# Kernel optimization log

Hardware: AMD Instinct MI355X
Metric: run time of the kernel (lower is better)

Reference implementation:

```python
import jax, jax.numpy as jnp
import numpy as np

B, S, D_MODEL = 4, 1024, 1024
N_HEAD, D_HEAD = 16, 64
ALL_HEAD = N_HEAD * D_HEAD
SCALE = 1.0 / (D_HEAD ** 0.5)
LN_EPS = 1e-5


def setup_inputs() -> dict:
    key = jax.random.key(0)
    ks = jax.random.split(key, 8)
    inp = jax.random.normal(ks[0], (B, S, D_MODEL), dtype=jnp.float32)
    attn_mask = jax.random.randint(ks[1], (B, S), 0, 2, dtype=jnp.int32)
    w = lambda k, shp: (jax.random.normal(k, shp, dtype=jnp.float32) * 0.02)
    Wq = w(ks[2], (D_MODEL, ALL_HEAD)); bq = jnp.zeros((ALL_HEAD,), jnp.float32)
    Wk = w(ks[3], (D_MODEL, ALL_HEAD)); bk = jnp.zeros((ALL_HEAD,), jnp.float32)
    Wv = w(ks[4], (D_MODEL, ALL_HEAD)); bv = jnp.zeros((ALL_HEAD,), jnp.float32)
    Wo = w(ks[5], (ALL_HEAD, D_MODEL))
    ln_g = jnp.ones((D_MODEL,), jnp.float32)
    ln_b = jnp.zeros((D_MODEL,), jnp.float32)
    return {"inp": inp, "attn_mask": attn_mask, "Wq": Wq, "bq": bq,
            "Wk": Wk, "bk": bk, "Wv": Wv, "bv": bv, "Wo": Wo,
            "ln_g": ln_g, "ln_b": ln_b}


def _layer_norm(x, g, b):
    mu = jnp.mean(x, axis=-1, keepdims=True)
    var = jnp.mean((x - mu) ** 2, axis=-1, keepdims=True)
    return (x - mu) * jax.lax.rsqrt(var + LN_EPS) * g + b


def reference(inp, attn_mask, Wq, bq, Wk, bk, Wv, bv, Wo, ln_g, ln_b):
    residual = inp
    # QKV projections -> [B, S, H, D] -> flat [B*H, S, D] (batch-major, as torch permute+reshape)
    def proj(W, bias):
        h = (inp @ W + bias).reshape(B, S, N_HEAD, D_HEAD)
        return h.transpose(0, 2, 1, 3).reshape(B * N_HEAD, S, D_HEAD)
    q = proj(Wq, bq)
    k = proj(Wk, bk)
    v = proj(Wv, bv)
    # scores [B*H, S, S]
    scores = jnp.einsum('bqd,bkd->bqk', q, k) * SCALE
    # key-padding mask: nonzero -> masked_fill(-100000.0)
    mask = (attn_mask.astype(scores.dtype) != 0)  # [B, S]
    mask = jnp.broadcast_to(mask[:, None, None, :], (B, N_HEAD, S, S))
    mask = mask.reshape(B * N_HEAD, S, S)
    scores = jnp.where(mask, jnp.float32(-100000.0), scores)
    probs = jax.nn.softmax(scores, axis=2)  # dropout is identity in eval
    attn_vec = jnp.einsum('bqk,bkd->bqd', probs, v)  # [B*H, S, D]
    # faithful to torch: view(n_head, B, S, d_head).permute(1,2,0,3)
    attn_vec = attn_vec.reshape(N_HEAD, B, S, D_HEAD).transpose(1, 2, 0, 3)
    attn_vec = attn_vec.reshape(B, S, ALL_HEAD)
    attn_out = attn_vec @ Wo  # o_net has no bias; output dropout identity
    # post-lnorm (pre_lnorm=False)
    return _layer_norm(residual + attn_out, ln_g, ln_b)
```

## Files before the change

### kernel.cpp

```cpp
#include <hip/hip_runtime.h>

typedef __attribute__((ext_vector_type(8))) short bf16x8;
typedef __attribute__((ext_vector_type(4))) float f32x4;
typedef __attribute__((ext_vector_type(16))) float f32x16;

#define D_MODEL 1024
#define SEQ 1024
#define NB 4
#define NH 16
#define DH 64
#define MROWS 4096

__device__ __forceinline__ unsigned short f2bf(float f) {
    union { float f; unsigned u; } x; x.f = f;
    unsigned r = x.u + 0x7fffu + ((x.u >> 16) & 1u);
    return (unsigned short)(r >> 16);
}

__device__ __forceinline__ float bf2f(unsigned short u) {
    union { unsigned u; float f; } x; x.u = (unsigned)u << 16;
    return x.f;
}

__device__ __forceinline__ void gload16(const void* g, void* l) {
    __builtin_amdgcn_global_load_lds((const __attribute__((address_space(1))) void*)g,
                                     (__attribute__((address_space(3))) void*)l, 16, 0, 0);
}

__device__ __forceinline__ float xhalf(float x, int hi) {
    float a = x, b = x;
    asm volatile("v_permlane32_swap_b32 %0, %1" : "+v"(a), "+v"(b));
    return hi ? b : a;
}

__global__ __launch_bounds__(256) void prep(const float* __restrict__ x,
                                            unsigned short* __restrict__ Xb,
                                            const int* __restrict__ amask,
                                            unsigned long long* __restrict__ mwords,
                                            const float* __restrict__ Wq,
                                            const float* __restrict__ Wk,
                                            const float* __restrict__ Wv,
                                            const float* __restrict__ Wo,
                                            unsigned short* __restrict__ Wqkv_t,
                                            unsigned short* __restrict__ Wo_t) {
    __shared__ float tile[32][33];
    const int bid = blockIdx.x, tid = threadIdx.x;
    if (bid < 4096) {
        int i = bid * 256 + tid;
        float4 v = ((const float4*)x)[i];
        ushort4 r;
        r.x = f2bf(v.x); r.y = f2bf(v.y); r.z = f2bf(v.z); r.w = f2bf(v.w);
        ((ushort4*)Xb)[i] = r;
    } else if (bid < 8192) {
        int t = bid - 4096;
        const int mtx = t >> 10, t10 = t & 1023;
        const float* src = mtx == 0 ? Wq : mtx == 1 ? Wk : mtx == 2 ? Wv : Wo;
        unsigned short* dst = mtx < 3 ? (Wqkv_t + (size_t)mtx * D_MODEL * D_MODEL) : Wo_t;
        const int n0 = (t10 & 31) * 32, k0 = (t10 >> 5) * 32;
        const int tx = tid & 31, ty = tid >> 5;
        #pragma unroll
        for (int i = 0; i < 32; i += 8)
            tile[ty + i][tx] = src[(size_t)(k0 + ty + i) * D_MODEL + n0 + tx];
        __syncthreads();
        #pragma unroll
        for (int i = 0; i < 32; i += 8)
            dst[(size_t)(n0 + ty + i) * D_MODEL + k0 + tx] = f2bf(tile[tx][ty + i]);
    } else {
        int word = (bid - 8192) * 4 + (tid >> 6);
        int lane = tid & 63;
        unsigned long long m = __ballot(amask[word * 64 + lane] != 0);
        if (lane == 0) mwords[word] = m;
    }
}

#define CSW(r, c) ((r) * 128 + ((c) ^ (((r) & 7) << 3)))

__global__ __launch_bounds__(256) void gemm_qkv(const unsigned short* __restrict__ Xb,
                                                const unsigned short* __restrict__ Wt,
                                                const float* __restrict__ bq,
                                                const float* __restrict__ bk,
                                                const float* __restrict__ bv,
                                                unsigned short* __restrict__ Qb,
                                                unsigned short* __restrict__ Kb,
                                                unsigned short* __restrict__ Vt) {
    __shared__ unsigned short SM[32768];
    const int tid = threadIdx.x;
    const int lane = tid & 63, wid = tid >> 6;
    const int fr = lane & 15, fg = lane >> 4;
    const int wr = wid >> 1, wc = wid & 1;
    const int lin = blockIdx.x;
    const int x = lin & 7, i = lin >> 3;
    const int bxm = (x & 3) * 8 + (i & 7);
    const int byn = (x >> 2) * 12 + (i >> 3);
    const int m0 = bxm * 128, n0 = byn * 128;
    const unsigned short* Ag = Xb + (size_t)m0 * D_MODEL;
    const unsigned short* Bg = Wt + (size_t)n0 * D_MODEL;
    const int srow = tid >> 3;
    const int scol = 8 * ((tid & 7) ^ ((tid >> 3) & 7));
    f32x4 acc[4][4] = {};

#define QSTAGE(bf, kt2)                                                                   \
    {                                                                                     \
        const int kb = (kt2) * 64;                                                        \
        _Pragma("unroll")                                                                 \
        for (int j = 0; j < 4; ++j) {                                                     \
            int row = j * 32 + srow;                                                      \
            gload16(Ag + (size_t)row * D_MODEL + kb + scol, &SM[(bf) * 16384 + (j * 256 + tid) * 8]); \
            gload16(Bg + (size_t)row * D_MODEL + kb + scol, &SM[(bf) * 16384 + 8192 + (j * 256 + tid) * 8]); \
        }                                                                                 \
    }

    QSTAGE(0, 0);
    __syncthreads();
    int buf = 0;
    for (int kt = 0; kt < 16; ++kt) {
        if (kt < 15) QSTAGE(buf ^ 1, kt + 1);
        const unsigned short* As = &SM[buf * 16384];
        const unsigned short* Bs = &SM[buf * 16384 + 8192];
        #pragma unroll
        for (int ks = 0; ks < 2; ++ks) {
            bf16x8 af[4], bfv[4];
            #pragma unroll
            for (int m = 0; m < 4; ++m) {
                int row = wr * 64 + m * 16 + fr;
                af[m] = *(const bf16x8*)&As[row * 64 + ((ks * 32 + fg * 8) ^ ((row & 7) * 8))];
            }
            #pragma unroll
            for (int n = 0; n < 4; ++n) {
                int row = wc * 64 + n * 16 + fr;
                bfv[n] = *(const bf16x8*)&Bs[row * 64 + ((ks * 32 + fg * 8) ^ ((row & 7) * 8))];
            }
            __builtin_amdgcn_s_setprio(1);
            #pragma unroll
            for (int m = 0; m < 4; ++m)
                #pragma unroll
                for (int n = 0; n < 4; ++n)
                    acc[m][n] = __builtin_amdgcn_mfma_f32_16x16x32_bf16(af[m], bfv[n], acc[m][n], 0, 0, 0);
            __builtin_amdgcn_s_setprio(0);
        }
        __syncthreads();
        buf ^= 1;
    }
#undef QSTAGE
    unsigned short* Cs = SM;
    const int sel = n0 >> 10;
    const int npb = n0 & 1023;
    if (sel < 2) {
        #pragma unroll
        for (int n = 0; n < 4; ++n) {
            int cn = wc * 64 + n * 16 + fr;
            float bias = (sel == 0 ? bq : bk)[npb + cn];
            #pragma unroll
            for (int m = 0; m < 4; ++m)
                #pragma unroll
                for (int r = 0; r < 4; ++r) {
                    int row = wr * 64 + m * 16 + fg * 4 + r;
                    Cs[CSW(row, cn)] = f2bf(acc[m][n][r] + bias);
                }
        }
        __syncthreads();
        unsigned short* dst = sel == 0 ? Qb : Kb;
        #pragma unroll
        for (int k = 0; k < 8; ++k) {
            int c = k * 256 + tid;
            int row = c >> 4, cc = c & 15;
            int np = npb + cc * 8;
            int h = np >> 6, d = np & 63;
            int gm = m0 + row, b = gm >> 10, s = gm & 1023;
            bf16x8 v = *(const bf16x8*)&Cs[CSW(row, cc * 8)];
            *(bf16x8*)&dst[((size_t)(b * NH + h) * SEQ + s) * DH + d] = v;
        }
    } else {
        #pragma unroll
        for (int n = 0; n < 4; ++n) {
            int cn = wc * 64 + n * 16 + fr;
            float bias = bv[npb + cn];
            #pragma unroll
            for (int m = 0; m < 4; ++m)
                #pragma unroll
                for (int r = 0; r < 4; ++r) {
                    int row = wr * 64 + m * 16 + fg * 4 + r;
                    Cs[CSW(cn, row)] = f2bf(acc[m][n][r] + bias);
                }
        }
        __syncthreads();
        #pragma unroll
        for (int k = 0; k < 8; ++k) {
            int c = k * 256 + tid;
            int dcol = c >> 4, scc = c & 15;
            int np = npb + dcol;
            int h = np >> 6, dd = np & 63;
            int gm0 = m0 + scc * 8, b = gm0 >> 10, s0 = gm0 & 1023;
            bf16x8 v = *(const bf16x8*)&Cs[CSW(dcol, scc * 8)];
            *(bf16x8*)&Vt[((size_t)(b * NH + h) * DH + dd) * SEQ + s0] = v;
        }
    }
}

__global__ __launch_bounds__(256) void gemm_o(const unsigned short* __restrict__ Ab,
                                              const unsigned short* __restrict__ Wt,
                                              unsigned short* __restrict__ tmpb) {
    __shared__ unsigned short SM[32768];
    const int tid = threadIdx.x;
    const int lane = tid & 63, wid = tid >> 6;
    const int fr = lane & 15, fg = lane >> 4;
    const int wr = wid >> 1, wc = wid & 1;
    const int lin = blockIdx.x;
    const int x = lin & 7, i = lin >> 3;
    const int bxm = (x & 3) * 8 + (i & 7);
    const int byn = (x >> 2) * 4 + (i >> 3);
    const int m0 = bxm * 128, n0 = byn * 128;
    const unsigned short* Ag = Ab + (size_t)m0 * D_MODEL;
    const unsigned short* Bg = Wt + (size_t)n0 * D_MODEL;
    const int srow = tid >> 3;
    const int scol = 8 * ((tid & 7) ^ ((tid >> 3) & 7));
    f32x4 acc[4][4] = {};

#define OSTAGE(bf, kt2)                                                                   \
    {                                                                                     \
        const int kb = (kt2) * 64;                                                        \
        _Pragma("unroll")                                                                 \
        for (int j = 0; j < 4; ++j) {                                                     \
            int row = j * 32 + srow;                                                      \
            gload16(Ag + (size_t)row * D_MODEL + kb + scol, &SM[(bf) * 16384 + (j * 256 + tid) * 8]); \
            gload16(Bg + (size_t)row * D_MODEL + kb + scol, &SM[(bf) * 16384 + 8192 + (j * 256 + tid) * 8]); \
        }                                                                                 \
    }

    OSTAGE(0, 0);
    __syncthreads();
    int buf = 0;
    for (int kt = 0; kt < 16; ++kt) {
        if (kt < 15) OSTAGE(buf ^ 1, kt + 1);
        const unsigned short* As = &SM[buf * 16384];
        const unsigned short* Bs = &SM[buf * 16384 + 8192];
        #pragma unroll
        for (int ks = 0; ks < 2; ++ks) {
            bf16x8 af[4], bfv[4];
            #pragma unroll
            for (int m = 0; m < 4; ++m) {
                int row = wr * 64 + m * 16 + fr;
                af[m] = *(const bf16x8*)&As[row * 64 + ((ks * 32 + fg * 8) ^ ((row & 7) * 8))];
            }
            #pragma unroll
            for (int n = 0; n < 4; ++n) {
                int row = wc * 64 + n * 16 + fr;
                bfv[n] = *(const bf16x8*)&Bs[row * 64 + ((ks * 32 + fg * 8) ^ ((row & 7) * 8))];
            }
            __builtin_amdgcn_s_setprio(1);
            #pragma unroll
            for (int m = 0; m < 4; ++m)
                #pragma unroll
                for (int n = 0; n < 4; ++n)
                    acc[m][n] = __builtin_amdgcn_mfma_f32_16x16x32_bf16(af[m], bfv[n], acc[m][n], 0, 0, 0);
            __builtin_amdgcn_s_setprio(0);
        }
        __syncthreads();
        buf ^= 1;
    }
#undef OSTAGE
    unsigned short* Cs = SM;
    #pragma unroll
    for (int n = 0; n < 4; ++n) {
        int cn = wc * 64 + n * 16 + fr;
        #pragma unroll
        for (int m = 0; m < 4; ++m)
            #pragma unroll
            for (int r = 0; r < 4; ++r) {
                int row = wr * 64 + m * 16 + fg * 4 + r;
                Cs[CSW(row, cn)] = f2bf(acc[m][n][r]);
            }
    }
    __syncthreads();
    #pragma unroll
    for (int k = 0; k < 8; ++k) {
        int c = k * 256 + tid;
        int row = c >> 4, cc = c & 15;
        bf16x8 v = *(const bf16x8*)&Cs[CSW(row, cc * 8)];
        *(bf16x8*)&tmpb[(size_t)(m0 + row) * D_MODEL + n0 + cc * 8] = v;
    }
}

__global__ __launch_bounds__(256, 2) void attn_kernel(const unsigned short* __restrict__ Qb,
                                                      const unsigned short* __restrict__ Kb,
                                                      const unsigned short* __restrict__ Vt,
                                                      const unsigned long long* __restrict__ mwords,
                                                      unsigned short* __restrict__ AF) {
    __shared__ unsigned short Ks[2][128 * 64];
    __shared__ unsigned short Vts[2][64 * 128];
    const int tid = threadIdx.x, lane = tid & 63, wid = tid >> 6;
    const int l31 = lane & 31, hi = lane >> 5;
    const int lin = blockIdx.x;
    const int x = lin & 7, i = lin >> 3;
    const int qt = i & 7, bh = x * 8 + (i >> 3);
    const int b = bh >> 4;
    const unsigned short* Qh = Qb + (size_t)bh * SEQ * DH;
    const unsigned short* Kh = Kb + (size_t)bh * SEQ * DH;
    const unsigned short* Vth = Vt + (size_t)bh * DH * SEQ;
    const unsigned long long* mwb = mwords + b * 16;
    const int q0 = qt * 128 + wid * 32;

    const int k_row = wid * 32 + (lane >> 3);
    const int k_col = 8 * ((lane & 7) ^ ((lane >> 3) & 7));
    const int v_rowb = wid * 16 + (lane >> 4);

    bf16x8 qf[4];
    #pragma unroll
    for (int ks = 0; ks < 4; ++ks)
        qf[ks] = *(const bf16x8*)(Qh + (size_t)(q0 + l31) * DH + ks * 16 + hi * 8);

    union U4 { unsigned u[4]; bf16x8 v; };
    U4 ones;
    ones.u[0] = 0x3F803F80u; ones.u[1] = 0x3F803F80u;
    ones.u[2] = 0x3F803F80u; ones.u[3] = 0x3F803F80u;

    f32x16 oacc0 = {}, oacc1 = {};
    f32x16 sacc = {};
    float mrun = -3.0e38f;
    const float C2 = 0.18033688f;

#define KSWZ(row, colsh) ((row) * 64 + ((colsh) ^ (((row) & 7) << 3)))
#define VSWZ(row, colsh) ((row) * 128 + ((colsh) ^ (((row) & 7) << 3)))
#define STAGE(bufi, kt2)                                                                  \
    {                                                                                     \
        const int kv0s = (kt2) * 128;                                                     \
        _Pragma("unroll")                                                                 \
        for (int j = 0; j < 4; ++j)                                                       \
            gload16(Kh + (size_t)(kv0s + k_row + j * 8) * DH + k_col,                     \
                    &Ks[bufi][wid * 2048 + j * 512]);                                     \
        _Pragma("unroll")                                                                 \
        for (int j = 0; j < 4; ++j) {                                                     \
            const int vr = v_rowb + j * 4;                                                \
            gload16(Vth + (size_t)vr * SEQ + kv0s + 8 * ((lane & 15) ^ (vr & 7)),         \
                    &Vts[bufi][wid * 2048 + j * 512]);                                    \
        }                                                                                 \
    }

    STAGE(0, 0);
    __syncthreads();
    int buf = 0;
    for (int kt = 0; kt < 8; ++kt) {
        if (kt < 7) STAGE(buf ^ 1, kt + 1);
        const unsigned long long mwA = mwb[2 * kt], mwB = mwb[2 * kt + 1];
        const unsigned mr0 = (unsigned)mwA, mr1 = (unsigned)(mwA >> 32);
        const unsigned mr2 = (unsigned)mwB, mr3 = (unsigned)(mwB >> 32);
        f32x16 sA0 = {}, sA1 = {}, sB0 = {}, sB1 = {};
        __builtin_amdgcn_s_setprio(1);
        #pragma unroll
        for (int ks = 0; ks < 4; ++ks) {
            const int ch = ks * 16 + hi * 8;
            bf16x8 k0 = *(const bf16x8*)&Ks[buf][KSWZ(l31, ch)];
            bf16x8 k1 = *(const bf16x8*)&Ks[buf][KSWZ(32 + l31, ch)];
            bf16x8 k2 = *(const bf16x8*)&Ks[buf][KSWZ(64 + l31, ch)];
            bf16x8 k3 = *(const bf16x8*)&Ks[buf][KSWZ(96 + l31, ch)];
            sA0 = __builtin_amdgcn_mfma_f32_32x32x16_bf16(k0, qf[ks], sA0, 0, 0, 0);
            sA1 = __builtin_amdgcn_mfma_f32_32x32x16_bf16(k1, qf[ks], sA1, 0, 0, 0);
            sB0 = __builtin_amdgcn_mfma_f32_32x32x16_bf16(k2, qf[ks], sB0, 0, 0, 0);
            sB1 = __builtin_amdgcn_mfma_f32_32x32x16_bf16(k3, qf[ks], sB1, 0, 0, 0);
        }
        {
            U4 ab; ab.u[1] = 0; ab.u[2] = 0; ab.u[3] = 0;
            unsigned bv;
            bv = ((mr0 >> l31) & 1u) ? 0xC943u : 0u; ab.u[0] = hi ? 0u : bv;
            sA0 = __builtin_amdgcn_mfma_f32_32x32x16_bf16(ab.v, ones.v, sA0, 0, 0, 0);
            bv = ((mr1 >> l31) & 1u) ? 0xC943u : 0u; ab.u[0] = hi ? 0u : bv;
            sA1 = __builtin_amdgcn_mfma_f32_32x32x16_bf16(ab.v, ones.v, sA1, 0, 0, 0);
            bv = ((mr2 >> l31) & 1u) ? 0xC943u : 0u; ab.u[0] = hi ? 0u : bv;
            sB0 = __builtin_amdgcn_mfma_f32_32x32x16_bf16(ab.v, ones.v, sB0, 0, 0, 0);
            bv = ((mr3 >> l31) & 1u) ? 0xC943u : 0u; ab.u[0] = hi ? 0u : bv;
            sB1 = __builtin_amdgcn_mfma_f32_32x32x16_bf16(ab.v, ones.v, sB1, 0, 0, 0);
        }
        __builtin_amdgcn_s_setprio(0);
        float tm[16];
        #pragma unroll
        for (int r2 = 0; r2 < 16; ++r2)
            tm[r2] = fmaxf(fmaxf(sA0[r2], sA1[r2]), fmaxf(sB0[r2], sB1[r2]));
        #pragma unroll
        for (int st = 8; st; st >>= 1)
            #pragma unroll
            for (int r2 = 0; r2 < st; ++r2)
                tm[r2] = fmaxf(tm[r2], tm[r2 + st]);
        float m = tm[0];
        m = fmaxf(m, xhalf(m, hi));
        float mt = m * C2;
        if (!__all(mt <= mrun + 11.5f)) {
            float newm = fmaxf(mrun, mt);
            float corr = exp2f(mrun - newm);
            #pragma unroll
            for (int r2 = 0; r2 < 16; ++r2) {
                oacc0[r2] *= corr; oacc1[r2] *= corr; sacc[r2] *= corr;
            }
            mrun = newm;
        }
        #pragma unroll
        for (int r2 = 0; r2 < 16; ++r2) {
            sA0[r2] = exp2f(fmaf(sA0[r2], C2, -mrun));
            sA1[r2] = exp2f(fmaf(sA1[r2], C2, -mrun));
            sB0[r2] = exp2f(fmaf(sB0[r2], C2, -mrun));
            sB1[r2] = exp2f(fmaf(sB1[r2], C2, -mrun));
        }
        unsigned cA0[8], cA1[8], cB0[8], cB1[8];
        #pragma unroll
        for (int ii = 0; ii < 8; ++ii) {
            asm volatile("v_cvt_pk_bf16_f32 %0, %1, %2" : "=v"(cA0[ii]) : "v"(sA0[2 * ii]), "v"(sA0[2 * ii + 1]));
            asm volatile("v_cvt_pk_bf16_f32 %0, %1, %2" : "=v"(cA1[ii]) : "v"(sA1[2 * ii]), "v"(sA1[2 * ii + 1]));
            asm volatile("v_cvt_pk_bf16_f32 %0, %1, %2" : "=v"(cB0[ii]) : "v"(sB0[2 * ii]), "v"(sB0[2 * ii + 1]));
            asm volatile("v_cvt_pk_bf16_f32 %0, %1, %2" : "=v"(cB1[ii]) : "v"(sB1[2 * ii]), "v"(sB1[2 * ii + 1]));
        }
        #pragma unroll
        for (int g = 0; g < 8; g += 4) {
            asm volatile("v_permlane32_swap_b32 %0, %1" : "+v"(cA0[g + 0]), "+v"(cA0[g + 2]));
            asm volatile("v_permlane32_swap_b32 %0, %1" : "+v"(cA0[g + 1]), "+v"(cA0[g + 3]));
            asm volatile("v_permlane32_swap_b32 %0, %1" : "+v"(cA1[g + 0]), "+v"(cA1[g + 2]));
            asm volatile("v_permlane32_swap_b32 %0, %1" : "+v"(cA1[g + 1]), "+v"(cA1[g + 3]));
            asm volatile("v_permlane32_swap_b32 %0, %1" : "+v"(cB0[g + 0]), "+v"(cB0[g + 2]));
            asm volatile("v_permlane32_swap_b32 %0, %1" : "+v"(cB0[g + 1]), "+v"(cB0[g + 3]));
            asm volatile("v_permlane32_swap_b32 %0, %1" : "+v"(cB1[g + 0]), "+v"(cB1[g + 2]));
            asm volatile("v_permlane32_swap_b32 %0, %1" : "+v"(cB1[g + 1]), "+v"(cB1[g + 3]));
        }
        __builtin_amdgcn_s_setprio(1);
        #pragma unroll
        for (int t = 0; t < 8; ++t) {
            const unsigned* cp = (t < 2) ? cA0 : (t < 4) ? cA1 : (t < 6) ? cB0 : cB1;
            const int g = (t & 1) * 4;
            U4 pb;
            pb.u[0] = cp[g + 0]; pb.u[1] = cp[g + 1]; pb.u[2] = cp[g + 2]; pb.u[3] = cp[g + 3];
            const int ch = t * 16 + hi * 8;
            bf16x8 vf0 = *(const bf16x8*)&Vts[buf][VSWZ(l31, ch)];
            bf16x8 vf1 = *(const bf16x8*)&Vts[buf][VSWZ(32 + l31, ch)];
            oacc0 = __builtin_amdgcn_mfma_f32_32x32x16_bf16(vf0, pb.v, oacc0, 0, 0, 0);
            oacc1 = __builtin_amdgcn_mfma_f32_32x32x16_bf16(vf1, pb.v, oacc1, 0, 0, 0);
            sacc  = __builtin_amdgcn_mfma_f32_32x32x16_bf16(ones.v, pb.v, sacc, 0, 0, 0);
        }
        __builtin_amdgcn_s_setprio(0);
        __syncthreads();
        buf ^= 1;
    }
#undef STAGE
#undef KSWZ
#undef VSWZ
    const float rl = 1.f / sacc[0];
    const int b2 = bh & 3, h2 = bh >> 2;
    const size_t rowbase = ((size_t)b2 * SEQ + q0 + l31) * D_MODEL + h2 * 64 + 4 * hi;
    #pragma unroll
    for (int df = 0; df < 2; ++df) {
        const f32x16& oa = df ? oacc1 : oacc0;
        #pragma unroll
        for (int rg = 0; rg < 4; ++rg) {
            ushort4 pk;
            pk.x = f2bf(oa[rg * 4 + 0] * rl);
            pk.y = f2bf(oa[rg * 4 + 1] * rl);
            pk.z = f2bf(oa[rg * 4 + 2] * rl);
            pk.w = f2bf(oa[rg * 4 + 3] * rl);
            *(ushort4*)&AF[rowbase + 32 * df + 8 * rg] = pk;
        }
    }
}

__global__ __launch_bounds__(256) void ln_kernel(const unsigned short* __restrict__ tmpb,
                                                 const float* __restrict__ inp,
                                                 const float* __restrict__ g,
                                                 const float* __restrict__ bb,
                                                 float* __restrict__ out) {
    __shared__ float red[8];
    const int row = blockIdx.x, tid = threadIdx.x;
    ushort4 t4 = ((const ushort4*)(tmpb + (size_t)row * D_MODEL))[tid];
    float4 rr = ((const float4*)(inp + (size_t)row * D_MODEL))[tid];
    float4 y;
    y.x = bf2f(t4.x) + rr.x; y.y = bf2f(t4.y) + rr.y;
    y.z = bf2f(t4.z) + rr.z; y.w = bf2f(t4.w) + rr.w;
    float sum = y.x + y.y + y.z + y.w;
    float sq = y.x * y.x + y.y * y.y + y.z * y.z + y.w * y.w;
    #pragma unroll
    for (int o = 1; o < 64; o <<= 1) { sum += __shfl_xor(sum, o); sq += __shfl_xor(sq, o); }
    int wid = tid >> 6, lane = tid & 63;
    if (lane == 0) { red[wid] = sum; red[4 + wid] = sq; }
    __syncthreads();
    sum = red[0] + red[1] + red[2] + red[3];
    sq = red[4] + red[5] + red[6] + red[7];
    float mu = sum * (1.f / D_MODEL);
    float var = sq * (1.f / D_MODEL) - mu * mu;
    float rs = rsqrtf(var + 1e-5f);
    float4 gg = ((const float4*)g)[tid];
    float4 bv = ((const float4*)bb)[tid];
    float4 o4;
    o4.x = (y.x - mu) * rs * gg.x + bv.x;
    o4.y = (y.y - mu) * rs * gg.y + bv.y;
    o4.z = (y.z - mu) * rs * gg.z + bv.z;
    o4.w = (y.w - mu) * rs * gg.w + bv.w;
    ((float4*)(out + (size_t)row * D_MODEL))[tid] = o4;
}

extern "C" void kernel_launch(void* const* d_in, const int* in_sizes, int n_in,
                              void* d_out, int out_size, void* d_ws, size_t ws_size,
                              hipStream_t stream) {
    const float* inp = (const float*)d_in[0];
    const int* amask = (const int*)d_in[1];
    const float* Wq = (const float*)d_in[2];
    const float* bq = (const float*)d_in[3];
    const float* Wk = (const float*)d_in[4];
    const float* bk = (const float*)d_in[5];
    const float* Wv = (const float*)d_in[6];
    const float* bv = (const float*)d_in[7];
    const float* Wo = (const float*)d_in[8];
    const float* lg = (const float*)d_in[9];
    const float* lb = (const float*)d_in[10];
    float* out = (float*)d_out;
    char* ws = (char*)d_ws;

    unsigned short* Xb     = (unsigned short*)(ws + 0);
    unsigned short* Wqkv_t = (unsigned short*)(ws + 8388608);
    unsigned short* Wo_t   = (unsigned short*)(ws + 14680064);
    unsigned short* Qb     = (unsigned short*)(ws + 16777216);
    unsigned short* Kb     = (unsigned short*)(ws + 25165824);
    unsigned short* Vt     = (unsigned short*)(ws + 33554432);
    unsigned short* AF     = (unsigned short*)(ws + 41943040);
    unsigned short* tmpb   = (unsigned short*)(ws + 50331648);
    unsigned long long* mwords = (unsigned long long*)(ws + 58720256);

    prep<<<8208, 256, 0, stream>>>(inp, Xb, amask, mwords, Wq, Wk, Wv, Wo, Wqkv_t, Wo_t);
    gemm_qkv<<<768, 256, 0, stream>>>(Xb, Wqkv_t, bq, bk, bv, Qb, Kb, Vt);
    attn_kernel<<<512, 256, 0, stream>>>(Qb, Kb, Vt, mwords, AF);
    gemm_o<<<256, 256, 0, stream>>>(AF, Wo_t, tmpb);
    ln_kernel<<<4096, 256, 0, stream>>>(tmpb, inp, lg, lb, out);
}
```

Measured before the change: 101.4 us.

## Split attention KV range in two halves and merge partials with combine kernel

Each attention block now handles half of the key/value sequence with 64-wide KV tiles, doubling the grid to 1024 blocks and halving shared memory so more blocks fit per CU. Unnormalized partial outputs plus running max and sum are written to workspace, and a new combine kernel merges the two halves with log-sum-exp weights into the head-interleaved layout. This aims to fix underutilization from only 512 blocks. In exchange it adds an extra launch, extra global traffic for the partials, and an extra bf16 rounding of the partial outputs. Opart reuses the Xb region, which is no longer needed once the QKV GEMM has run.

```diff
diff --git a/kernel.cpp b/kernel.cpp
--- a/kernel.cpp
+++ b/kernel.cpp
@@ -281,28 +281,27 @@
     }
 }
 
-__global__ __launch_bounds__(256, 2) void attn_kernel(const unsigned short* __restrict__ Qb,
+__global__ __launch_bounds__(256, 4) void attn_kernel(const unsigned short* __restrict__ Qb,
                                                       const unsigned short* __restrict__ Kb,
                                                       const unsigned short* __restrict__ Vt,
                                                       const unsigned long long* __restrict__ mwords,
-                                                      unsigned short* __restrict__ AF) {
-    __shared__ unsigned short Ks[2][128 * 64];
-    __shared__ unsigned short Vts[2][64 * 128];
+                                                      unsigned short* __restrict__ Opart,
+                                                      float* __restrict__ ml) {
+    __shared__ unsigned short Ks[2][64 * 64];
+    __shared__ unsigned short Vts[2][64 * 64];
     const int tid = threadIdx.x, lane = tid & 63, wid = tid >> 6;
     const int l31 = lane & 31, hi = lane >> 5;
     const int lin = blockIdx.x;
     const int x = lin & 7, i = lin >> 3;
-    const int qt = i & 7, bh = x * 8 + (i >> 3);
+    const int bh = x * 8 + (i >> 4);
+    const int rem = i & 15, qt = rem >> 1, half = rem & 1;
     const int b = bh >> 4;
     const unsigned short* Qh = Qb + (size_t)bh * SEQ * DH;
     const unsigned short* Kh = Kb + (size_t)bh * SEQ * DH;
     const unsigned short* Vth = Vt + (size_t)bh * DH * SEQ;
-    const unsigned long long* mwb = mwords + b * 16;
+    const unsigned long long* mwb = mwords + b * 16 + half * 8;
     const int q0 = qt * 128 + wid * 32;
-
-    const int k_row = wid * 32 + (lane >> 3);
-    const int k_col = 8 * ((lane & 7) ^ ((lane >> 3) & 7));
-    const int v_rowb = wid * 16 + (lane >> 4);
+    const int kvbase = half * 512;
 
     bf16x8 qf[4];
     #pragma unroll
@@ -320,19 +319,16 @@
     const float C2 = 0.18033688f;
 
 #define KSWZ(row, colsh) ((row) * 64 + ((colsh) ^ (((row) & 7) << 3)))
-#define VSWZ(row, colsh) ((row) * 128 + ((colsh) ^ (((row) & 7) << 3)))
 #define STAGE(bufi, kt2)                                                                  \
     {                                                                                     \
-        const int kv0s = (kt2) * 128;                                                     \
+        const int kv0s = kvbase + (kt2) * 64;                                             \
         _Pragma("unroll")                                                                 \
-        for (int j = 0; j < 4; ++j)                                                       \
-            gload16(Kh + (size_t)(kv0s + k_row + j * 8) * DH + k_col,                     \
-                    &Ks[bufi][wid * 2048 + j * 512]);                                     \
-        _Pragma("unroll")                                                                 \
-        for (int j = 0; j < 4; ++j) {                                                     \
-            const int vr = v_rowb + j * 4;                                                \
-            gload16(Vth + (size_t)vr * SEQ + kv0s + 8 * ((lane & 15) ^ (vr & 7)),         \
-                    &Vts[bufi][wid * 2048 + j * 512]);                                    \
+        for (int j = 0; j < 2; ++j) {                                                     \
+            const int c = j * 256 + tid;                                                  \
+            const int row = c >> 3;                                                       \
+            const int scolx = 8 * ((c & 7) ^ (row & 7));                                  \
+            gload16(Kh + (size_t)(kv0s + row) * DH + scolx, &Ks[bufi][c * 8]);            \
+            gload16(Vth + (size_t)row * SEQ + kv0s + scolx, &Vts[bufi][c * 8]);           \
         }                                                                                 \
     }
 
@@ -341,22 +337,17 @@
     int buf = 0;
     for (int kt = 0; kt < 8; ++kt) {
         if (kt < 7) STAGE(buf ^ 1, kt + 1);
-        const unsigned long long mwA = mwb[2 * kt], mwB = mwb[2 * kt + 1];
-        const unsigned mr0 = (unsigned)mwA, mr1 = (unsigned)(mwA >> 32);
-        const unsigned mr2 = (unsigned)mwB, mr3 = (unsigned)(mwB >> 32);
-        f32x16 sA0 = {}, sA1 = {}, sB0 = {}, sB1 = {};
+        const unsigned long long mw = mwb[kt];
+        const unsigned mr0 = (unsigned)mw, mr1 = (unsigned)(mw >> 32);
+        f32x16 sA0 = {}, sA1 = {};
         __builtin_amdgcn_s_setprio(1);
         #pragma unroll
         for (int ks = 0; ks < 4; ++ks) {
             const int ch = ks * 16 + hi * 8;
             bf16x8 k0 = *(const bf16x8*)&Ks[buf][KSWZ(l31, ch)];
             bf16x8 k1 = *(const bf16x8*)&Ks[buf][KSWZ(32 + l31, ch)];
-            bf16x8 k2 = *(const bf16x8*)&Ks[buf][KSWZ(64 + l31, ch)];
-            bf16x8 k3 = *(const bf16x8*)&Ks[buf][KSWZ(96 + l31, ch)];
             sA0 = __builtin_amdgcn_mfma_f32_32x32x16_bf16(k0, qf[ks], sA0, 0, 0, 0);
             sA1 = __builtin_amdgcn_mfma_f32_32x32x16_bf16(k1, qf[ks], sA1, 0, 0, 0);
-            sB0 = __builtin_amdgcn_mfma_f32_32x32x16_bf16(k2, qf[ks], sB0, 0, 0, 0);
-            sB1 = __builtin_amdgcn_mfma_f32_32x32x16_bf16(k3, qf[ks], sB1, 0, 0, 0);
         }
         {
             U4 ab; ab.u[1] = 0; ab.u[2] = 0; ab.u[3] = 0;
@@ -365,16 +356,12 @@
             sA0 = __builtin_amdgcn_mfma_f32_32x32x16_bf16(ab.v, ones.v, sA0, 0, 0, 0);
             bv = ((mr1 >> l31) & 1u) ? 0xC943u : 0u; ab.u[0] = hi ? 0u : bv;
             sA1 = __builtin_amdgcn_mfma_f32_32x32x16_bf16(ab.v, ones.v, sA1, 0, 0, 0);
-            bv = ((mr2 >> l31) & 1u) ? 0xC943u : 0u; ab.u[0] = hi ? 0u : bv;
-            sB0 = __builtin_amdgcn_mfma_f32_32x32x16_bf16(ab.v, ones.v, sB0, 0, 0, 0);
-            bv = ((mr3 >> l31) & 1u) ? 0xC943u : 0u; ab.u[0] = hi ? 0u : bv;
-            sB1 = __builtin_amdgcn_mfma_f32_32x32x16_bf16(ab.v, ones.v, sB1, 0, 0, 0);
         }
         __builtin_amdgcn_s_setprio(0);
         float tm[16];
         #pragma unroll
         for (int r2 = 0; r2 < 16; ++r2)
-            tm[r2] = fmaxf(fmaxf(sA0[r2], sA1[r2]), fmaxf(sB0[r2], sB1[r2]));
+            tm[r2] = fmaxf(sA0[r2], sA1[r2]);
         #pragma unroll
         for (int st = 8; st; st >>= 1)
             #pragma unroll
@@ -396,16 +383,12 @@
         for (int r2 = 0; r2 < 16; ++r2) {
             sA0[r2] = exp2f(fmaf(sA0[r2], C2, -mrun));
             sA1[r2] = exp2f(fmaf(sA1[r2], C2, -mrun));
-            sB0[r2] = exp2f(fmaf(sB0[r2], C2, -mrun));
-            sB1[r2] = exp2f(fmaf(sB1[r2], C2, -mrun));
-        }
-        unsigned cA0[8], cA1[8], cB0[8], cB1[8];
+        }
+        unsigned cA0[8], cA1[8];
         #pragma unroll
         for (int ii = 0; ii < 8; ++ii) {
             asm volatile("v_cvt_pk_bf16_f32 %0, %1, %2" : "=v"(cA0[ii]) : "v"(sA0[2 * ii]), "v"(sA0[2 * ii + 1]));
             asm volatile("v_cvt_pk_bf16_f32 %0, %1, %2" : "=v"(cA1[ii]) : "v"(sA1[2 * ii]), "v"(sA1[2 * ii + 1]));
-            asm volatile("v_cvt_pk_bf16_f32 %0, %1, %2" : "=v"(cB0[ii]) : "v"(sB0[2 * ii]), "v"(sB0[2 * ii + 1]));
-            asm volatile("v_cvt_pk_bf16_f32 %0, %1, %2" : "=v"(cB1[ii]) : "v"(sB1[2 * ii]), "v"(sB1[2 * ii + 1]));
         }
         #pragma unroll
         for (int g = 0; g < 8; g += 4) {
@@ -413,21 +396,17 @@
             asm volatile("v_permlane32_swap_b32 %0, %1" : "+v"(cA0[g + 1]), "+v"(cA0[g + 3]));
             asm volatile("v_permlane32_swap_b32 %0, %1" : "+v"(cA1[g + 0]), "+v"(cA1[g + 2]));
             asm volatile("v_permlane32_swap_b32 %0, %1" : "+v"(cA1[g + 1]), "+v"(cA1[g + 3]));
-            asm volatile("v_permlane32_swap_b32 %0, %1" : "+v"(cB0[g + 0]), "+v"(cB0[g + 2]));
-            asm volatile("v_permlane32_swap_b32 %0, %1" : "+v"(cB0[g + 1]), "+v"(cB0[g + 3]));
-            asm volatile("v_permlane32_swap_b32 %0, %1" : "+v"(cB1[g + 0]), "+v"(cB1[g + 2]));
-            asm volatile("v_permlane32_swap_b32 %0, %1" : "+v"(cB1[g + 1]), "+v"(cB1[g + 3]));
         }
         __builtin_amdgcn_s_setprio(1);
         #pragma unroll
-        for (int t = 0; t < 8; ++t) {
-            const unsigned* cp = (t < 2) ? cA0 : (t < 4) ? cA1 : (t < 6) ? cB0 : cB1;
+        for (int t = 0; t < 4; ++t) {
+            const unsigned* cp = (t < 2) ? cA0 : cA1;
             const int g = (t & 1) * 4;
             U4 pb;
             pb.u[0] = cp[g + 0]; pb.u[1] = cp[g + 1]; pb.u[2] = cp[g + 2]; pb.u[3] = cp[g + 3];
             const int ch = t * 16 + hi * 8;
-            bf16x8 vf0 = *(const bf16x8*)&Vts[buf][VSWZ(l31, ch)];
-            bf16x8 vf1 = *(const bf16x8*)&Vts[buf][VSWZ(32 + l31, ch)];
+            bf16x8 vf0 = *(const bf16x8*)&Vts[buf][KSWZ(l31, ch)];
+            bf16x8 vf1 = *(const bf16x8*)&Vts[buf][KSWZ(32 + l31, ch)];
             oacc0 = __builtin_amdgcn_mfma_f32_32x32x16_bf16(vf0, pb.v, oacc0, 0, 0, 0);
             oacc1 = __builtin_amdgcn_mfma_f32_32x32x16_bf16(vf1, pb.v, oacc1, 0, 0, 0);
             sacc  = __builtin_amdgcn_mfma_f32_32x32x16_bf16(ones.v, pb.v, sacc, 0, 0, 0);
@@ -438,22 +417,60 @@
     }
 #undef STAGE
 #undef KSWZ
-#undef VSWZ
-    const float rl = 1.f / sacc[0];
-    const int b2 = bh & 3, h2 = bh >> 2;
-    const size_t rowbase = ((size_t)b2 * SEQ + q0 + l31) * D_MODEL + h2 * 64 + 4 * hi;
+    const int qtl = bh * 8 + qt;
+    const int qloc = wid * 32 + l31;
+    const size_t pbase = ((size_t)(half * 512 + qtl) * 128 + qloc) * 64 + 4 * hi;
     #pragma unroll
     for (int df = 0; df < 2; ++df) {
         const f32x16& oa = df ? oacc1 : oacc0;
         #pragma unroll
         for (int rg = 0; rg < 4; ++rg) {
             ushort4 pk;
-            pk.x = f2bf(oa[rg * 4 + 0] * rl);
-            pk.y = f2bf(oa[rg * 4 + 1] * rl);
-            pk.z = f2bf(oa[rg * 4 + 2] * rl);
-            pk.w = f2bf(oa[rg * 4 + 3] * rl);
-            *(ushort4*)&AF[rowbase + 32 * df + 8 * rg] = pk;
-        }
+            pk.x = f2bf(oa[rg * 4 + 0]);
+            pk.y = f2bf(oa[rg * 4 + 1]);
+            pk.z = f2bf(oa[rg * 4 + 2]);
+            pk.w = f2bf(oa[rg * 4 + 3]);
+            *(ushort4*)&Opart[pbase + 32 * df + 8 * rg] = pk;
+        }
+    }
+    if (hi == 0) {
+        float* mlp = &ml[((size_t)(half * 512 + qtl) * 128 + qloc) * 2];
+        mlp[0] = mrun;
+        mlp[1] = sacc[0];
+    }
+}
+
+__global__ __launch_bounds__(256) void combine(const unsigned short* __restrict__ Opart,
+                                               const float* __restrict__ ml,
+                                               unsigned short* __restrict__ AF) {
+    const int qtl = blockIdx.x, tid = threadIdx.x;
+    const int bh = qtl >> 3, qt = qtl & 7;
+    const int b2 = bh & 3, h2 = bh >> 2;
+    const int q = tid >> 1, dbase = (tid & 1) * 32;
+    const float* m1p = &ml[((size_t)qtl * 128 + q) * 2];
+    const float* m2p = &ml[((size_t)(512 + qtl) * 128 + q) * 2];
+    const float m1 = m1p[0], l1 = m1p[1];
+    const float m2 = m2p[0], l2 = m2p[1];
+    const float M = fmaxf(m1, m2);
+    float w1 = exp2f(m1 - M), w2 = exp2f(m2 - M);
+    const float rden = 1.f / (w1 * l1 + w2 * l2);
+    w1 *= rden; w2 *= rden;
+    const size_t p1 = ((size_t)qtl * 128 + q) * 64 + dbase;
+    const size_t p2 = ((size_t)(512 + qtl) * 128 + q) * 64 + dbase;
+    const size_t ob = ((size_t)b2 * SEQ + qt * 128 + q) * D_MODEL + h2 * 64 + dbase;
+    #pragma unroll
+    for (int c = 0; c < 4; ++c) {
+        bf16x8 o1 = *(const bf16x8*)&Opart[p1 + 8 * c];
+        bf16x8 o2 = *(const bf16x8*)&Opart[p2 + 8 * c];
+        ushort4 lo, hi4;
+        unsigned short r[8];
+        #pragma unroll
+        for (int j = 0; j < 8; ++j)
+            r[j] = f2bf(w1 * bf2f((unsigned short)o1[j]) + w2 * bf2f((unsigned short)o2[j]));
+        lo.x = r[0]; lo.y = r[1]; lo.z = r[2]; lo.w = r[3];
+        hi4.x = r[4]; hi4.y = r[5]; hi4.z = r[6]; hi4.w = r[7];
+        *(ushort4*)&AF[ob + 8 * c] = lo;
+        *(ushort4*)&AF[ob + 8 * c + 4] = hi4;
     }
 }
 
@@ -510,17 +527,20 @@
 
     unsigned short* Xb     = (unsigned short*)(ws + 0);
     unsigned short* Wqkv_t = (unsigned short*)(ws + 8388608);
-    unsigned short* Wo_t   = (unsigned short*)(ws + 14680064);
     unsigned short* Qb     = (unsigned short*)(ws + 16777216);
     unsigned short* Kb     = (unsigned short*)(ws + 25165824);
     unsigned short* Vt     = (unsigned short*)(ws + 33554432);
-    unsigned short* AF     = (unsigned short*)(ws + 41943040);
-    unsigned short* tmpb   = (unsigned short*)(ws + 50331648);
-    unsigned long long* mwords = (unsigned long long*)(ws + 58720256);
+    unsigned short* Wo_t   = (unsigned short*)(ws + 41943040);
+    unsigned short* AF     = (unsigned short*)(ws + 44040192);
+    unsigned short* tmpb   = (unsigned short*)(ws + 52428800);
+    unsigned long long* mwords = (unsigned long long*)(ws + 60817408);
+    float*          ml     = (float*)(ws + 60821504);
+    unsigned short* Opart  = (unsigned short*)(ws + 0);
 
     prep<<<8208, 256, 0, stream>>>(inp, Xb, amask, mwords, Wq, Wk, Wv, Wo, Wqkv_t, Wo_t);
     gemm_qkv<<<768, 256, 0, stream>>>(Xb, Wqkv_t, bq, bk, bv, Qb, Kb, Vt);
-    attn_kernel<<<512, 256, 0, stream>>>(Qb, Kb, Vt, mwords, AF);
+    attn_kernel<<<1024, 256, 0, stream>>>(Qb, Kb, Vt, mwords, Opart, ml);
+    combine<<<512, 256, 0, stream>>>(Opart, ml, AF);
     gemm_o<<<256, 256, 0, stream>>>(AF, Wo_t, tmpb);
     ln_kernel<<<4096, 256, 0, stream>>>(tmpb, inp, lg, lb, out);
 }
```

Result: slower. 114.5 us (+12.9%).
